# Kernel tuning notes

Hardware: AMD Instinct MI355X
Metric: run time of the kernel (lower is better)

Reference implementation:

```python
import jax, jax.numpy as jnp
import numpy as np

ALPHA = 0.2  # LeakyReLU negative slope (init arg alpha)


def setup_inputs() -> dict:
    key = jax.random.key(0)
    k1, k2, k3 = jax.random.split(key, 3)
    B, N, F_in, F_out = 8, 2048, 256, 256
    inp = jax.random.normal(k1, (B, N, F_in), dtype=jnp.float32)
    adj = jnp.ones((B, N, N), dtype=jnp.float32)  # unused by the module's forward
    # xavier_uniform with gain=1.414
    gain = 1.414
    bW = gain * np.sqrt(6.0 / (F_in + F_out))
    W = jax.random.uniform(k2, (F_in, F_out), minval=-bW, maxval=bW, dtype=jnp.float32)
    ba = gain * np.sqrt(6.0 / (2 * F_out + 1))
    a = jax.random.uniform(k3, (2 * F_out, 1), minval=-ba, maxval=ba, dtype=jnp.float32)
    return {"inp": inp, "adj": adj, "W": W, "a": a}


def reference(inp, adj, W, a):
    # inp: [B, N, F_in]; W: [F_in, F_out]; a: [2*F_out, 1]. adj is unused (as in source).
    F_out = W.shape[1]
    h = jnp.matmul(inp, W)  # [B, N, F_out]
    # e[b,i,j] = leakyrelu(a1 . h_i + a2 . h_j)  (equivalent to the repeat+cat+matmul)
    a1 = a[:F_out, 0]
    a2 = a[F_out:, 0]
    s1 = jnp.einsum('bnf,f->bn', h, a1)  # [B, N]
    s2 = jnp.einsum('bnf,f->bn', h, a2)  # [B, N]
    e = jax.nn.leaky_relu(s1[:, :, None] + s2[:, None, :], negative_slope=ALPHA)  # [B, N, N]
    # global per-batch min-max normalization, then affine *30 - 20
    mn = jnp.min(e, axis=(1, 2), keepdims=True)
    mx = jnp.max(e, axis=(1, 2), keepdims=True)
    e = (e - mn) / (mx - mn) * 30.0 - 20.0
    attention = jax.nn.sigmoid(e)  # dropout p=0 / eval: identity
    h_prime = jnp.matmul(attention, h)  # [B, N, F_out]
    h_prime = jax.nn.elu(h_prime)  # concat=True branch
    return h_prime, attention
```

## Files before the change

kernel.cpp:

```cpp
#include <hip/hip_runtime.h>
#include <stdint.h>

#define B_   8
#define N_   2048
#define F_   256
#define BN_  (B_ * N_)
#define ALPHA_ 0.2f

typedef __attribute__((ext_vector_type(8))) short  short8;
typedef __attribute__((ext_vector_type(4))) float  f32x4;

__device__ __forceinline__ unsigned short f2bf(float x) {
  uint32_t u = __float_as_uint(x);
  uint32_t r = (u + 0x7fffu + ((u >> 16) & 1u)) >> 16;
  return (unsigned short)r;
}

__device__ __forceinline__ void async_load16(const void* g, void* l) {
  __builtin_amdgcn_global_load_lds(
      (const __attribute__((address_space(1))) uint32_t*)g,
      (__attribute__((address_space(3))) uint32_t*)l, 16, 0, 0);
}

__global__ void k_cvt_inp(const float* __restrict__ x, unsigned short* __restrict__ y) {
  int idx = (blockIdx.x * 256 + threadIdx.x) * 4;
  float4 v = *(const float4*)(x + idx);
  ushort4 p;
  p.x = f2bf(v.x); p.y = f2bf(v.y); p.z = f2bf(v.z); p.w = f2bf(v.w);
  *(ushort4*)(y + idx) = p;
}

__global__ void k_cvt_w(const float* __restrict__ W, unsigned short* __restrict__ WT) {
  int k = blockIdx.x, n = threadIdx.x;
  WT[n * F_ + k] = f2bf(W[k * F_ + n]);
}

__launch_bounds__(256, 1)
__global__ void k_gemm1(const unsigned short* __restrict__ inpb,
                        const unsigned short* __restrict__ WT,
                        const float* __restrict__ avec,
                        unsigned short* __restrict__ hT,
                        float* __restrict__ s1g, float* __restrict__ s2g) {
  __shared__ __align__(16) unsigned short Atile[64 * 32];
  __shared__ __align__(16) unsigned short Btile[256 * 32];
  __shared__ float s1_lds[64], s2_lds[64];

  const int tid  = threadIdx.x;
  const int wave = tid >> 6, lane = tid & 63;
  const int n16  = lane & 15, quad = lane >> 4;
  const int i0   = blockIdx.x * 64;

  if (tid < 64) { s1_lds[tid] = 0.0f; s2_lds[tid] = 0.0f; }

  f32x4 acc[4][4];
  #pragma unroll
  for (int mt = 0; mt < 4; ++mt)
    #pragma unroll
    for (int nt = 0; nt < 4; ++nt) acc[mt][nt] = (f32x4){0.f, 0.f, 0.f, 0.f};

  for (int k0 = 0; k0 < F_; k0 += 32) {
    {
      int r = (wave << 4) + (lane >> 2);
      int p = lane & 3;
      async_load16(inpb + (size_t)(i0 + r) * F_ + k0 + p * 8,
                   (char*)Atile + wave * 1024);
    }
    #pragma unroll
    for (int g4 = 0; g4 < 4; ++g4) {
      int f = (wave << 6) + (g4 << 4) + (lane >> 2);
      int p = lane & 3;
      async_load16(WT + (size_t)f * F_ + k0 + p * 8,
                   (char*)Btile + wave * 4096 + g4 * 1024);
    }
    __syncthreads();

    short8 af[4], bf_[4];
    #pragma unroll
    for (int mt = 0; mt < 4; ++mt)
      af[mt] = *(const short8*)((const char*)Atile + ((mt * 16 + n16) * 64 + quad * 16));
    #pragma unroll
    for (int nt = 0; nt < 4; ++nt)
      bf_[nt] = *(const short8*)((const char*)Btile + ((wave * 64 + nt * 16 + n16) * 64 + quad * 16));
    #pragma unroll
    for (int mt = 0; mt < 4; ++mt)
      #pragma unroll
      for (int nt = 0; nt < 4; ++nt)
        acc[mt][nt] = __builtin_amdgcn_mfma_f32_16x16x32_bf16(af[mt], bf_[nt], acc[mt][nt], 0, 0, 0);
    __syncthreads();
  }

  float a1v[4], a2v[4];
  #pragma unroll
  for (int nt = 0; nt < 4; ++nt) {
    int f = (wave << 6) + (nt << 4) + n16;
    a1v[nt] = avec[f];
    a2v[nt] = avec[F_ + f];
  }
  #pragma unroll
  for (int mt = 0; mt < 4; ++mt) {
    float s1p[4] = {0, 0, 0, 0}, s2p[4] = {0, 0, 0, 0};
    #pragma unroll
    for (int nt = 0; nt < 4; ++nt) {
      int f  = (wave << 6) + (nt << 4) + n16;
      int ig = i0 + (mt << 4) + (quad << 2);
      ushort4 pk;
      pk.x = f2bf(acc[mt][nt][0]); pk.y = f2bf(acc[mt][nt][1]);
      pk.z = f2bf(acc[mt][nt][2]); pk.w = f2bf(acc[mt][nt][3]);
      *(ushort4*)(hT + (size_t)f * BN_ + ig) = pk;
      #pragma unroll
      for (int rg = 0; rg < 4; ++rg) {
        s1p[rg] = fmaf(acc[mt][nt][rg], a1v[nt], s1p[rg]);
        s2p[rg] = fmaf(acc[mt][nt][rg], a2v[nt], s2p[rg]);
      }
    }
    #pragma unroll
    for (int rg = 0; rg < 4; ++rg) {
      float v1 = s1p[rg], v2 = s2p[rg];
      #pragma unroll
      for (int off = 1; off < 16; off <<= 1) {
        v1 += __shfl_xor(v1, off);
        v2 += __shfl_xor(v2, off);
      }
      if (n16 == 0) {
        atomicAdd(&s1_lds[(mt << 4) + (quad << 2) + rg], v1);
        atomicAdd(&s2_lds[(mt << 4) + (quad << 2) + rg], v2);
      }
    }
  }
  __syncthreads();
  if (tid < 64) {
    s1g[i0 + tid] = s1_lds[tid];
    s2g[i0 + tid] = s2_lds[tid];
  }
}

__global__ void k_minmax(const float* __restrict__ s1, const float* __restrict__ s2,
                         float2* __restrict__ params) {
  int b = blockIdx.x, tid = threadIdx.x;
  float mn1 = 1e30f, mx1 = -1e30f, mn2 = 1e30f, mx2 = -1e30f;
  for (int i = tid; i < N_; i += 256) {
    float v1 = s1[b * N_ + i]; mn1 = fminf(mn1, v1); mx1 = fmaxf(mx1, v1);
    float v2 = s2[b * N_ + i]; mn2 = fminf(mn2, v2); mx2 = fmaxf(mx2, v2);
  }
  #pragma unroll
  for (int off = 1; off < 64; off <<= 1) {
    mn1 = fminf(mn1, __shfl_xor(mn1, off));
    mx1 = fmaxf(mx1, __shfl_xor(mx1, off));
    mn2 = fminf(mn2, __shfl_xor(mn2, off));
    mx2 = fmaxf(mx2, __shfl_xor(mx2, off));
  }
  __shared__ float red[4][4];
  int wave = tid >> 6, lane = tid & 63;
  if (lane == 0) { red[wave][0] = mn1; red[wave][1] = mx1; red[wave][2] = mn2; red[wave][3] = mx2; }
  __syncthreads();
  if (tid == 0) {
    for (int w = 1; w < 4; ++w) {
      mn1 = fminf(mn1, red[w][0]); mx1 = fmaxf(mx1, red[w][1]);
      mn2 = fminf(mn2, red[w][2]); mx2 = fmaxf(mx2, red[w][3]);
    }
    float smn = mn1 + mn2, smx = mx1 + mx2;
    float mn = fmaxf(smn, ALPHA_ * smn);
    float mx = fmaxf(smx, ALPHA_ * smx);
    float scale = 30.0f / (mx - mn);
    float bias  = -mn * scale - 20.0f;
    params[b] = make_float2(-scale, -bias);
  }
}

__launch_bounds__(256, 1)
__global__ void k_gemm2(const unsigned short* __restrict__ hT,
                        const float* __restrict__ s1, const float* __restrict__ s2,
                        const float2* __restrict__ params,
                        float* __restrict__ hprime,
                        float* __restrict__ att) {
  __shared__ __align__(16) unsigned short Atile[64 * 32];
  __shared__ __align__(16) unsigned short Btile[256 * 32];

  const int tid  = threadIdx.x;
  const int wave = tid >> 6, lane = tid & 63;
  const int n16  = lane & 15, quad = lane >> 4;
  const int blk  = blockIdx.x;
  const int b    = blk & 7;
  const int i0   = (blk >> 3) * 64;

  const float2 pb = params[b];
  const float uscale = pb.x, ubias = pb.y;

  const int r_att = tid >> 2;
  const int p_att = tid & 3;
  const float s1v = s1[b * N_ + i0 + r_att];
  const float* s2b = s2 + b * N_;
  float* attrow = att + ((size_t)(b * N_ + i0 + r_att)) * N_;

  f32x4 acc[4][4];
  #pragma unroll
  for (int mt = 0; mt < 4; ++mt)
    #pragma unroll
    for (int nt = 0; nt < 4; ++nt) acc[mt][nt] = (f32x4){0.f, 0.f, 0.f, 0.f};

  for (int k0 = 0; k0 < N_; k0 += 32) {
    #pragma unroll
    for (int g4 = 0; g4 < 4; ++g4) {
      int f = (wave << 6) + (g4 << 4) + (lane >> 2);
      int p = lane & 3;
      async_load16(hT + (size_t)f * BN_ + b * N_ + k0 + p * 8,
                   (char*)Btile + wave * 4096 + g4 * 1024);
    }

    float4 va = *(const float4*)(s2b + k0 + p_att * 8);
    float4 vb = *(const float4*)(s2b + k0 + p_att * 8 + 4);
    float v[8] = {va.x, va.y, va.z, va.w, vb.x, vb.y, vb.z, vb.w};
    short8 spk;
    #pragma unroll
    for (int jj = 0; jj < 8; ++jj) {
      float s = s1v + v[jj];
      float l = fmaxf(s, ALPHA_ * s);
      float u = fmaf(l, uscale, ubias);
      float p_ = __builtin_amdgcn_rcpf(1.0f + __expf(u));
      v[jj] = p_;
      spk[jj] = (short)f2bf(p_);
    }
    *(float4*)(attrow + k0 + p_att * 8)     = make_float4(v[0], v[1], v[2], v[3]);
    *(float4*)(attrow + k0 + p_att * 8 + 4) = make_float4(v[4], v[5], v[6], v[7]);
    *(short8*)((char*)Atile + tid * 16) = spk;
    __syncthreads();

    short8 af[4], bf_[4];
    #pragma unroll
    for (int mt = 0; mt < 4; ++mt)
      af[mt] = *(const short8*)((const char*)Atile + ((mt * 16 + n16) * 64 + quad * 16));
    #pragma unroll
    for (int nt = 0; nt < 4; ++nt)
      bf_[nt] = *(const short8*)((const char*)Btile + ((wave * 64 + nt * 16 + n16) * 64 + quad * 16));
    #pragma unroll
    for (int mt = 0; mt < 4; ++mt)
      #pragma unroll
      for (int nt = 0; nt < 4; ++nt)
        acc[mt][nt] = __builtin_amdgcn_mfma_f32_16x16x32_bf16(af[mt], bf_[nt], acc[mt][nt], 0, 0, 0);
    __syncthreads();
  }

  float* hp = hprime + ((size_t)(b * N_ + i0)) * F_;
  #pragma unroll
  for (int mt = 0; mt < 4; ++mt)
    #pragma unroll
    for (int nt = 0; nt < 4; ++nt) {
      int fcol = (wave << 6) + (nt << 4) + n16;
      int irow = (mt << 4) + (quad << 2);
      #pragma unroll
      for (int rg = 0; rg < 4; ++rg) {
        float x = acc[mt][nt][rg];
        float y = x > 0.0f ? x : (__expf(x) - 1.0f);
        hp[(size_t)(irow + rg) * F_ + fcol] = y;
      }
    }
}

extern "C" void kernel_launch(void* const* d_in, const int* in_sizes, int n_in,
                              void* d_out, int out_size, void* d_ws, size_t ws_size,
                              hipStream_t stream) {
  const float* inp  = (const float*)d_in[0];
  const float* W    = (const float*)d_in[2];
  const float* avec = (const float*)d_in[3];

  float* hprime = (float*)d_out;
  float* att    = (float*)d_out + (size_t)B_ * N_ * F_;

  char* ws = (char*)d_ws;
  unsigned short* inpb = (unsigned short*)ws;
  unsigned short* WT   = (unsigned short*)(ws + 8388608);
  unsigned short* hT   = (unsigned short*)(ws + 8388608 + 131072);
  float* s1            = (float*)(ws + 8388608 + 131072 + 8388608);
  float* s2            = s1 + BN_;
  float2* params       = (float2*)(s2 + BN_);

  k_cvt_inp<<<(BN_ * F_) / 1024, 256, 0, stream>>>(inp, inpb);
  k_cvt_w<<<F_, F_, 0, stream>>>(W, WT);
  k_gemm1<<<BN_ / 64, 256, 0, stream>>>(inpb, WT, avec, hT, s1, s2);
  k_minmax<<<B_, 256, 0, stream>>>(s1, s2, params);
  k_gemm2<<<256, 256, 0, stream>>>(hT, s1, s2, params, hprime, att);
}
```

Baseline: 308.2 us.

## Stage hT transpose through LDS and halve gemm2 row tile to double grid

In gemm1, the bf16 h tile is first written to an LDS transpose buffer and then stored to hT with coalesced 16-byte rows, instead of scattered 8-byte stores. In gemm2, the per-block row tile shrinks from 64 to 32 rows, the grid doubles to 512 blocks, and launch bounds allow two blocks per CU. The aim is to fill more of the GPU's CUs, since 256 blocks underuse them, and to overlap the attention writes. The cost is that each hT column tile is reloaded twice as often, with less MFMA work per B-tile load.

After: 289.3 us. 6.1% less time.

```diff
diff --git a/kernel.cpp b/kernel.cpp
--- a/kernel.cpp
+++ b/kernel.cpp
@@ -43,6 +43,7 @@
                         float* __restrict__ s1g, float* __restrict__ s2g) {
   __shared__ __align__(16) unsigned short Atile[64 * 32];
   __shared__ __align__(16) unsigned short Btile[256 * 32];
+  __shared__ __align__(16) unsigned short Trans[256 * 72];
   __shared__ float s1_lds[64], s2_lds[64];
 
   const int tid  = threadIdx.x;
@@ -89,6 +90,18 @@
     __syncthreads();
   }
 
+  #pragma unroll
+  for (int mt = 0; mt < 4; ++mt)
+    #pragma unroll
+    for (int nt = 0; nt < 4; ++nt) {
+      int f = (wave << 6) + (nt << 4) + n16;
+      int i = (mt << 4) + (quad << 2);
+      ushort4 pk;
+      pk.x = f2bf(acc[mt][nt][0]); pk.y = f2bf(acc[mt][nt][1]);
+      pk.z = f2bf(acc[mt][nt][2]); pk.w = f2bf(acc[mt][nt][3]);
+      *(ushort4*)(Trans + f * 72 + i) = pk;
+    }
+
   float a1v[4], a2v[4];
   #pragma unroll
   for (int nt = 0; nt < 4; ++nt) {
@@ -100,19 +113,12 @@
   for (int mt = 0; mt < 4; ++mt) {
     float s1p[4] = {0, 0, 0, 0}, s2p[4] = {0, 0, 0, 0};
     #pragma unroll
-    for (int nt = 0; nt < 4; ++nt) {
-      int f  = (wave << 6) + (nt << 4) + n16;
-      int ig = i0 + (mt << 4) + (quad << 2);
-      ushort4 pk;
-      pk.x = f2bf(acc[mt][nt][0]); pk.y = f2bf(acc[mt][nt][1]);
-      pk.z = f2bf(acc[mt][nt][2]); pk.w = f2bf(acc[mt][nt][3]);
-      *(ushort4*)(hT + (size_t)f * BN_ + ig) = pk;
+    for (int nt = 0; nt < 4; ++nt)
       #pragma unroll
       for (int rg = 0; rg < 4; ++rg) {
         s1p[rg] = fmaf(acc[mt][nt][rg], a1v[nt], s1p[rg]);
         s2p[rg] = fmaf(acc[mt][nt][rg], a2v[nt], s2p[rg]);
       }
-    }
     #pragma unroll
     for (int rg = 0; rg < 4; ++rg) {
       float v1 = s1p[rg], v2 = s2p[rg];
@@ -128,6 +134,14 @@
     }
   }
   __syncthreads();
+
+  #pragma unroll
+  for (int it = 0; it < 8; ++it) {
+    int f = it * 32 + wave * 8 + (lane >> 3);
+    int i = (lane & 7) * 8;
+    short8 v = *(const short8*)(Trans + f * 72 + i);
+    *(short8*)(hT + (size_t)f * BN_ + i0 + i) = v;
+  }
   if (tid < 64) {
     s1g[i0 + tid] = s1_lds[tid];
     s2g[i0 + tid] = s2_lds[tid];
@@ -167,13 +181,13 @@
   }
 }
 
-__launch_bounds__(256, 1)
+__launch_bounds__(256, 2)
 __global__ void k_gemm2(const unsigned short* __restrict__ hT,
                         const float* __restrict__ s1, const float* __restrict__ s2,
                         const float2* __restrict__ params,
                         float* __restrict__ hprime,
                         float* __restrict__ att) {
-  __shared__ __align__(16) unsigned short Atile[64 * 32];
+  __shared__ __align__(16) unsigned short Atile[32 * 32];
   __shared__ __align__(16) unsigned short Btile[256 * 32];
 
   const int tid  = threadIdx.x;
@@ -181,20 +195,20 @@
   const int n16  = lane & 15, quad = lane >> 4;
   const int blk  = blockIdx.x;
   const int b    = blk & 7;
-  const int i0   = (blk >> 3) * 64;
+  const int i0   = (blk >> 3) * 32;
 
   const float2 pb = params[b];
   const float uscale = pb.x, ubias = pb.y;
 
-  const int r_att = tid >> 2;
-  const int p_att = tid & 3;
+  const int r_att = tid >> 3;
+  const int c_att = tid & 7;
   const float s1v = s1[b * N_ + i0 + r_att];
   const float* s2b = s2 + b * N_;
   float* attrow = att + ((size_t)(b * N_ + i0 + r_att)) * N_;
 
-  f32x4 acc[4][4];
-  #pragma unroll
-  for (int mt = 0; mt < 4; ++mt)
+  f32x4 acc[2][4];
+  #pragma unroll
+  for (int mt = 0; mt < 2; ++mt)
     #pragma unroll
     for (int nt = 0; nt < 4; ++nt) acc[mt][nt] = (f32x4){0.f, 0.f, 0.f, 0.f};
 
@@ -207,33 +221,31 @@
                    (char*)Btile + wave * 4096 + g4 * 1024);
     }
 
-    float4 va = *(const float4*)(s2b + k0 + p_att * 8);
-    float4 vb = *(const float4*)(s2b + k0 + p_att * 8 + 4);
-    float v[8] = {va.x, va.y, va.z, va.w, vb.x, vb.y, vb.z, vb.w};
-    short8 spk;
-    #pragma unroll
-    for (int jj = 0; jj < 8; ++jj) {
+    float4 va = *(const float4*)(s2b + k0 + c_att * 4);
+    float v[4] = {va.x, va.y, va.z, va.w};
+    ushort4 spk;
+    #pragma unroll
+    for (int jj = 0; jj < 4; ++jj) {
       float s = s1v + v[jj];
       float l = fmaxf(s, ALPHA_ * s);
       float u = fmaf(l, uscale, ubias);
       float p_ = __builtin_amdgcn_rcpf(1.0f + __expf(u));
       v[jj] = p_;
-      spk[jj] = (short)f2bf(p_);
-    }
-    *(float4*)(attrow + k0 + p_att * 8)     = make_float4(v[0], v[1], v[2], v[3]);
-    *(float4*)(attrow + k0 + p_att * 8 + 4) = make_float4(v[4], v[5], v[6], v[7]);
-    *(short8*)((char*)Atile + tid * 16) = spk;
-    __syncthreads();
-
-    short8 af[4], bf_[4];
-    #pragma unroll
-    for (int mt = 0; mt < 4; ++mt)
+    }
+    spk.x = f2bf(v[0]); spk.y = f2bf(v[1]); spk.z = f2bf(v[2]); spk.w = f2bf(v[3]);
+    *(float4*)(attrow + k0 + c_att * 4) = make_float4(v[0], v[1], v[2], v[3]);
+    *(ushort4*)(Atile + tid * 4) = spk;
+    __syncthreads();
+
+    short8 af[2], bf_[4];
+    #pragma unroll
+    for (int mt = 0; mt < 2; ++mt)
       af[mt] = *(const short8*)((const char*)Atile + ((mt * 16 + n16) * 64 + quad * 16));
     #pragma unroll
     for (int nt = 0; nt < 4; ++nt)
       bf_[nt] = *(const short8*)((const char*)Btile + ((wave * 64 + nt * 16 + n16) * 64 + quad * 16));
     #pragma unroll
-    for (int mt = 0; mt < 4; ++mt)
+    for (int mt = 0; mt < 2; ++mt)
       #pragma unroll
       for (int nt = 0; nt < 4; ++nt)
         acc[mt][nt] = __builtin_amdgcn_mfma_f32_16x16x32_bf16(af[mt], bf_[nt], acc[mt][nt], 0, 0, 0);
@@ -242,7 +254,7 @@
 
   float* hp = hprime + ((size_t)(b * N_ + i0)) * F_;
   #pragma unroll
-  for (int mt = 0; mt < 4; ++mt)
+  for (int mt = 0; mt < 2; ++mt)
     #pragma unroll
     for (int nt = 0; nt < 4; ++nt) {
       int fcol = (wave << 6) + (nt << 4) + n16;
@@ -278,5 +290,5 @@
   k_cvt_w<<<F_, F_, 0, stream>>>(W, WT);
   k_gemm1<<<BN_ / 64, 256, 0, stream>>>(inpb, WT, avec, hT, s1, s2);
   k_minmax<<<B_, 256, 0, stream>>>(s1, s2, params);
-  k_gemm2<<<256, 256, 0, stream>>>(hT, s1, s2, params, hprime, att);
-}
+  k_gemm2<<<512, 256, 0, stream>>>(hT, s1, s2, params, hprime, att);
+}
```
